# Optimization experiments

Measured on AMD Instinct MI355X. Metric: run time of the kernel, lower is better.

Reference implementation:

```python
import jax, jax.numpy as jnp
import numpy as np

H = 512      # hidden_dim
OPS = 12     # num_ops
E = 112      # total_edges = num_cells * sum(i+2 for i in range(num_nodes)) = 8*14


def setup_inputs() -> dict:
    key = jax.random.key(0)
    ks = jax.random.split(key, 16)
    s = lambda k, shape: jax.random.normal(k, shape, dtype=jnp.float32) * 0.05
    return {
        "temperature": 1,
        "h0": s(ks[0], (2, H)),
        "c0": s(ks[1], (2, H)),
        "Wih0": s(ks[2], (4 * H, H)),
        "Whh0": s(ks[3], (4 * H, H)),
        "bih0": s(ks[4], (4 * H,)),
        "bhh0": s(ks[5], (4 * H,)),
        "Wih1": s(ks[6], (4 * H, H)),
        "Whh1": s(ks[7], (4 * H, H)),
        "bih1": s(ks[8], (4 * H,)),
        "bhh1": s(ks[9], (4 * H,)),
        "emb": s(ks[10], (OPS, H)),
        "cW1": s(ks[11], (E, H, H)),
        "cb1": s(ks[12], (E, H)),
        "cW2": s(ks[13], (E, H, OPS)),
        "cb2": s(ks[14], (E, OPS)),
    }


def _lstm_cell(x, h, c, Wih, Whh, bih, bhh):
    # PyTorch LSTM gate order: i, f, g, o
    gates = x @ Wih.T + bih + h @ Whh.T + bhh  # [4H]
    i, f, g, o = jnp.split(gates, 4)
    c2 = jax.nn.sigmoid(f) * c + jax.nn.sigmoid(i) * jnp.tanh(g)
    h2 = jax.nn.sigmoid(o) * jnp.tanh(c2)
    return h2, c2


def reference(temperature, h0, c0, Wih0, Whh0, bih0, bhh0,
              Wih1, Whh1, bih1, bhh1, emb, cW1, cb1, cW2, cb2):
    temp = jnp.asarray(temperature, jnp.float32)
    # Gumbel-max trick == torch Categorical sampling (fixed on-device noise)
    gumbel = jax.random.gumbel(jax.random.key(42), (E, OPS), dtype=jnp.float32)

    def step(carry, xs):
        h, c, prev_action = carry          # h, c: [2, H]
        idx, W1, b1, W2, b2, gnoise = xs
        x = jnp.where(idx == 0, jnp.zeros((H,), jnp.float32), emb[prev_action])
        h0n, c0n = _lstm_cell(x, h[0], c[0], Wih0, Whh0, bih0, bhh0)
        h1n, c1n = _lstm_cell(h0n, h[1], c[1], Wih1, Whh1, bih1, bhh1)
        hmlp = jax.nn.relu(h1n @ W1 + b1)   # controller hidden
        logits = (hmlp @ W2 + b2) / temp    # [OPS]
        logp = jax.nn.log_softmax(logits)
        action = jnp.argmax(logits + gnoise).astype(jnp.int32)
        lp = logp[action]
        ent = -jnp.sum(jnp.exp(logp) * logp)
        new_carry = (jnp.stack([h0n, h1n]), jnp.stack([c0n, c1n]), action)
        return new_carry, (action, lp, ent)

    init = (h0, c0, jnp.int32(0))
    xs = (jnp.arange(E), cW1, cb1, cW2, cb2, gumbel)
    _, (actions, log_probs, entropies) = jax.lax.scan(step, init, xs)
    return actions, log_probs, entropies
```

## Files before the change

### kernel.cpp

```cpp
#include <hip/hip_runtime.h>
#include <math.h>

#define H    512
#define OPS  12
#define E    112
#define NWG  128
#define NT   256

typedef unsigned long long u64;
typedef unsigned int u32x4 __attribute__((ext_vector_type(4)));

#define TW_HB0   0
#define TW_HB1   1024
#define TW_HMB   2048
#define TW_TOTAL 3072
#define WS_W1T_F (16 + 2 * TW_TOTAL)

__device__ __forceinline__ float sigf(float x) { return 1.f / (1.f + expf(-x)); }

__device__ __forceinline__ void threefry_42(unsigned x0, unsigned x1,
                                            unsigned& o0, unsigned& o1) {
  const unsigned k0 = 0u, k1 = 42u;
  const unsigned k2 = k0 ^ k1 ^ 0x1BD11BDAu;
  x0 += k0; x1 += k1;
#define TF_R(rot) { x0 += x1; x1 = (x1 << rot) | (x1 >> (32 - rot)); x1 ^= x0; }
  TF_R(13) TF_R(15) TF_R(26) TF_R(6)
  x0 += k1; x1 += k2 + 1u;
  TF_R(17) TF_R(29) TF_R(16) TF_R(24)
  x0 += k2; x1 += k0 + 2u;
  TF_R(13) TF_R(15) TF_R(26) TF_R(6)
  x0 += k0; x1 += k1 + 3u;
  TF_R(17) TF_R(29) TF_R(16) TF_R(24)
  x0 += k1; x1 += k2 + 4u;
  TF_R(13) TF_R(15) TF_R(26) TF_R(6)
  x0 += k2; x1 += k0 + 5u;
#undef TF_R
  o0 = x0; o1 = x1;
}

__device__ __forceinline__ float bits_to_gumbel(unsigned bits) {
  unsigned fb = (bits >> 9) | 0x3f800000u;
  float u = __uint_as_float(fb) - 1.0f;
  u = u + 1.17549435e-38f;
  u = fmaxf(1.17549435e-38f, u);
  return -logf(-logf(u));
}

__device__ __forceinline__ float decode_temp(const void* temp_p) {
  float tf = *(const float*)temp_p;
  float a = fabsf(tf);
  if (a > 1e-6f && a < 1e6f) return tf;
  int ti = *(const int*)temp_p;
  if (ti != 0 && ti > -1000000 && ti < 1000000) return (float)ti;
  double td = *(const double*)temp_p;
  double ad = fabs(td);
  if (ad > 1e-6 && ad < 1e6) return (float)td;
  return 1.0f;
}

__device__ __forceinline__ void tag_store(u64* p, unsigned tag, float f) {
  u64 v = ((u64)tag << 32) | (u64)__float_as_uint(f);
  __hip_atomic_store(p, v, __ATOMIC_RELAXED, __HIP_MEMORY_SCOPE_SYSTEM);
}
__device__ __forceinline__ void tag_poll2(const u64* p, unsigned tag,
                                          float& f0, float& f1) {
  u32x4 v;
  for (;;) {
    asm volatile("global_load_dwordx4 %0, %1, off sc0 sc1\n\t"
                 "s_waitcnt vmcnt(0)"
                 : "=&v"(v) : "v"(p) : "memory");
    if (v.y == tag && v.w == tag) break;
    __builtin_amdgcn_s_sleep(1);
  }
  f0 = __uint_as_float(v.x);
  f1 = __uint_as_float(v.z);
}

__global__ void k_init(u64* tw) {
  int t = blockIdx.x * blockDim.x + threadIdx.x;
  if (t < TW_TOTAL) tw[t] = 0ull;
}
__global__ void k_diag(float* out, float v) {
  if (threadIdx.x == 0 && blockIdx.x == 0) out[0] = v;
}

__global__ void __launch_bounds__(NT)
k_w1t(const float* __restrict__ cW1, float* __restrict__ w1t) {
  int t = blockIdx.x * NT + threadIdx.x;
  size_t e0 = (size_t)t * 4;
  int i = (int)(e0 >> 18);
  int rem = (int)(e0 & 262143);
  int k = rem >> 9, j = rem & 511;
  int b = j >> 4, jc = j & 15;
  float4 v = *(const float4*)(cW1 + e0);
  size_t dst = (((size_t)(i * 32 + b) * 512 + k) << 4) + jc;
  *(float4*)(w1t + dst) = v;
}

__global__ void __launch_bounds__(NT)
policy_persist(const void* temp_p,
               const float* __restrict__ h0_in, const float* __restrict__ c0_in,
               const float* __restrict__ Wih0,  const float* __restrict__ Whh0,
               const float* __restrict__ bih0,  const float* __restrict__ bhh0,
               const float* __restrict__ Wih1,  const float* __restrict__ Whh1,
               const float* __restrict__ bih1,  const float* __restrict__ bhh1,
               const float* __restrict__ emb,   const float* __restrict__ cW1,
               const float* __restrict__ cb1,   const float* __restrict__ cW2,
               const float* __restrict__ cb2,
               float* __restrict__ out, float* ws, int use_w1t) {
  __shared__ __align__(16) float h0full[H], shp1[H], hm[H];
  __shared__ float g0pre[16], g1bpre[16], g1loc[16];
  __shared__ float ewloc[12 * 16], b0loc[16], b1loc[16];
  __shared__ float gum[E * OPS];
  __shared__ float w1s[512 * 5];
  __shared__ float w2s[512 * 13];
  __shared__ float c0loc[4], c1loc[4];
  __shared__ float spart[4][4];
  __shared__ int s_act;

  const int tid = threadIdx.x;
  const int bid = blockIdx.x;
  const int j0  = bid * 4;
  const int cb  = (bid & 7) * 16 + (bid >> 3);
  const float invt = 1.f / decode_temp(temp_p);

  u64* HB0 = (u64*)(ws + 16) + TW_HB0;
  u64* HB1 = (u64*)(ws + 16) + TW_HB1;
  u64* HMB = (u64*)(ws + 16) + TW_HMB;
  const float* W1T = ws + WS_W1T_F;
  const int bb = cb >> 2, boff = (cb & 3) * 4;

  for (int p = tid; p < E * OPS; p += NT) {
    unsigned y0, y1;
    threefry_42(0u, (unsigned)p, y0, y1);
    gum[p] = bits_to_gumbel(y0 ^ y1);
  }
  for (int j = tid; j < H; j += NT) {
    h0full[j] = h0_in[j];
    shp1[j]   = h0_in[H + j];
  }
  if (tid < 192) {
    int a = tid / 16, ridx = tid % 16;
    int g = ridx >> 2, dj = ridx & 3;
    int row = g * H + j0 + dj;
    const float* er = emb + a * H;
    const float* wr = Wih0 + (size_t)row * H;
    float acc = 0.f;
    for (int k = 0; k < H; k += 4) {
      float4 e4 = *(const float4*)(er + k);
      float4 w4 = *(const float4*)(wr + k);
      acc += e4.x * w4.x + e4.y * w4.y + e4.z * w4.z + e4.w * w4.w;
    }
    ewloc[tid] = acc;
  }
  if (tid < 16) {
    int g = tid >> 2, dj = tid & 3;
    int row = g * H + j0 + dj;
    b0loc[tid] = bih0[row] + bhh0[row];
    b1loc[tid] = bih1[row] + bhh1[row];
  }
  if (tid < 4) {
    c0loc[tid] = c0_in[j0 + tid];
    c1loc[tid] = c0_in[H + j0 + tid];
  }
  __syncthreads();

  {
    int rowidx = tid >> 3, lane = tid & 7;
    int cell = rowidx >> 4, ridx = rowidx & 15;
    int g = ridx >> 2, dj = ridx & 3;
    int row = g * H + j0 + dj;
    const float* wr = (cell ? Whh1 : Whh0) + (size_t)row * H + lane * 64;
    const float* hv = (cell ? shp1 : h0full) + lane * 64;
    float acc = 0.f;
#pragma unroll
    for (int k = 0; k < 64; k += 4) {
      float4 w4 = *(const float4*)(wr + k);
      acc += w4.x * hv[k] + w4.y * hv[k + 1] + w4.z * hv[k + 2] + w4.w * hv[k + 3];
    }
    acc += __shfl_xor(acc, 1);
    acc += __shfl_xor(acc, 2);
    acc += __shfl_xor(acc, 4);
    if (lane == 0) {
      if (cell == 0) g0pre[ridx] = acc + b0loc[ridx];
      else           g1bpre[ridx] = acc;
    }
    float4 r0, r1;
    if (use_w1t) {
      const float* wt = W1T + (((size_t)bb * 512) << 4) + boff;
      r0 = *(const float4*)(wt + ((size_t)tid << 4));
      r1 = *(const float4*)(wt + ((size_t)(tid + 256) << 4));
    } else {
      const float* wb = cW1 + (size_t)cb * 4;
      r0 = *(const float4*)(wb + (size_t)tid * H);
      r1 = *(const float4*)(wb + (size_t)(tid + 256) * H);
    }
    int k0 = tid * 5, k1 = (tid + 256) * 5;
    w1s[k0] = r0.x; w1s[k0 + 1] = r0.y; w1s[k0 + 2] = r0.z; w1s[k0 + 3] = r0.w;
    w1s[k1] = r1.x; w1s[k1 + 1] = r1.y; w1s[k1 + 2] = r1.z; w1s[k1 + 3] = r1.w;
  }
  __syncthreads();

#pragma unroll 1
  for (int i = 0; i < E; ++i) {
    const int p = i & 1;
    const unsigned tg = (unsigned)(i + 1);

    if (i > 0) {
      const int q = (i - 1) & 1;
      int t2 = tid * 2;
      tag_poll2(&HMB[q * 512 + t2], (unsigned)i, hm[t2], hm[t2 + 1]);
      __syncthreads();
      if (tid < 64) {
        float lg[OPS];
#pragma unroll
        for (int o = 0; o < OPS; ++o) lg[o] = 0.f;
#pragma unroll
        for (int jj = 0; jj < 8; ++jj) {
          int j = jj * 64 + tid;
          float hmv = hm[j];
          const float* w2r = &w2s[j * 13];
#pragma unroll
          for (int o = 0; o < OPS; ++o) lg[o] += hmv * w2r[o];
        }
#pragma unroll
        for (int s = 1; s < 64; s <<= 1) {
#pragma unroll
          for (int o = 0; o < OPS; ++o) lg[o] += __shfl_xor(lg[o], s);
        }
#pragma unroll
        for (int o = 0; o < OPS; ++o) lg[o] = (lg[o] + cb2[(i - 1) * OPS + o]) * invt;
        float mx = lg[0];
#pragma unroll
        for (int o = 1; o < OPS; ++o) mx = fmaxf(mx, lg[o]);
        float se = 0.f;
#pragma unroll
        for (int o = 0; o < OPS; ++o) se += expf(lg[o] - mx);
        float logZ = mx + logf(se);
        float best = -1e30f; int act = 0;
#pragma unroll
        for (int o = 0; o < OPS; ++o) {
          float v = lg[o] + gum[(i - 1) * OPS + o];
          if (v > best) { best = v; act = o; }
        }
        if (tid == 0) {
          s_act = act;
          if (bid == 0) {
            float lp = lg[act] - logZ;
            float ent = 0.f;
            for (int o = 0; o < OPS; ++o) {
              float l2 = lg[o] - logZ;
              ent -= expf(l2) * l2;
            }
            out[i - 1]         = (float)act;
            out[E + i - 1]     = lp;
            out[2 * E + i - 1] = ent;
          }
        }
      }
    }

    if (tid < 4) {
      int a = (i > 0) ? s_act : -1;
      float gi = g0pre[tid];
      float gf = g0pre[4 + tid];
      float gg = g0pre[8 + tid];
      float go = g0pre[12 + tid];
      if (a >= 0) {
        gi += ewloc[a * 16 + tid];
        gf += ewloc[a * 16 + 4 + tid];
        gg += ewloc[a * 16 + 8 + tid];
        go += ewloc[a * 16 + 12 + tid];
      }
      float cn = sigf(gf) * c0loc[tid] + sigf(gi) * tanhf(gg);
      c0loc[tid] = cn;
      tag_store(&HB0[p * 512 + j0 + tid], tg, sigf(go) * tanhf(cn));
    }

    {
      int t2 = tid * 2;
      tag_poll2(&HB0[p * 512 + t2], tg, h0full[t2], h0full[t2 + 1]);
    }
    __syncthreads();

    {
      int ridx = tid >> 4, lane = tid & 15;
      int g = ridx >> 2, dj = ridx & 3;
      int row = g * H + j0 + dj;
      const float* wr = Wih1 + (size_t)row * H + lane * 32;
      const float* hv = h0full + lane * 32;
      float acc = 0.f;
#pragma unroll
      for (int k = 0; k < 32; k += 4) {
        float4 w4 = *(const float4*)(wr + k);
        acc += w4.x * hv[k] + w4.y * hv[k + 1] + w4.z * hv[k + 2] + w4.w * hv[k + 3];
      }
      acc += __shfl_xor(acc, 1);
      acc += __shfl_xor(acc, 2);
      acc += __shfl_xor(acc, 4);
      acc += __shfl_xor(acc, 8);
      if (lane == 0) g1loc[ridx] = acc + g1bpre[ridx] + b1loc[ridx];
    }
    __syncthreads();

    if (tid < 4) {
      float gi = g1loc[tid];
      float gf = g1loc[4 + tid];
      float gg = g1loc[8 + tid];
      float go = g1loc[12 + tid];
      float cn = sigf(gf) * c1loc[tid] + sigf(gi) * tanhf(gg);
      c1loc[tid] = cn;
      tag_store(&HB1[p * 512 + j0 + tid], tg, sigf(go) * tanhf(cn));
    }

    float4 v0, v1;
    if (i + 1 < E) {
      if (use_w1t) {
        const float* wt = W1T + (((size_t)((i + 1) * 32 + bb) * 512) << 4) + boff;
        v0 = *(const float4*)(wt + ((size_t)tid << 4));
        v1 = *(const float4*)(wt + ((size_t)(tid + 256) << 4));
      } else {
        const float* wb = cW1 + (size_t)(i + 1) * H * H + (size_t)cb * 4;
        v0 = *(const float4*)(wb + (size_t)tid * H);
        v1 = *(const float4*)(wb + (size_t)(tid + 256) * H);
      }
    }
    if (tid < 128) {
      int ridx = tid >> 3, lane = tid & 7;
      int g = ridx >> 2, dj = ridx & 3;
      int row = g * H + j0 + dj;
      const float* wr = Whh0 + (size_t)row * H + lane * 64;
      const float* hv = h0full + lane * 64;
      float acc = 0.f;
#pragma unroll
      for (int k = 0; k < 64; k += 4) {
        float4 w4 = *(const float4*)(wr + k);
        acc += w4.x * hv[k] + w4.y * hv[k + 1] + w4.z * hv[k + 2] + w4.w * hv[k + 3];
      }
      acc += __shfl_xor(acc, 1);
      acc += __shfl_xor(acc, 2);
      acc += __shfl_xor(acc, 4);
      if (lane == 0) g0pre[ridx] = acc + b0loc[ridx];
    }
    {
      const float* wsrc = cW2 + (size_t)i * H * OPS;
#pragma unroll
      for (int r = 0; r < 6; ++r) {
        int q = tid + 256 * r;
        float4 v = *(const float4*)(wsrc + 4 * q);
        int f = 4 * q;
        w2s[(f / 12) * 13 + (f % 12)]             = v.x;
        w2s[((f + 1) / 12) * 13 + ((f + 1) % 12)] = v.y;
        w2s[((f + 2) / 12) * 13 + ((f + 2) % 12)] = v.z;
        w2s[((f + 3) / 12) * 13 + ((f + 3) % 12)] = v.w;
      }
    }

    {
      int t2 = tid * 2;
      tag_poll2(&HB1[p * 512 + t2], tg, shp1[t2], shp1[t2 + 1]);
    }
    __syncthreads();

    {
      int wv = tid >> 6, ln = tid & 63;
      int jl = ln & 3, ks = ln >> 2;
      int kbase = wv * 128 + ks * 8;
      float acc = 0.f;
#pragma unroll
      for (int t = 0; t < 8; ++t) {
        int k = kbase + t;
        acc += shp1[k] * w1s[k * 5 + jl];
      }
      acc += __shfl_xor(acc, 4);
      acc += __shfl_xor(acc, 8);
      acc += __shfl_xor(acc, 16);
      acc += __shfl_xor(acc, 32);
      if (ln < 4) spart[wv][ln] = acc;
    }
    __syncthreads();
    if (tid < 4) {
      float s = spart[0][tid] + spart[1][tid] + spart[2][tid] + spart[3][tid];
      s += cb1[(size_t)i * H + cb * 4 + tid];
      tag_store(&HMB[p * 512 + cb * 4 + tid], tg, fmaxf(s, 0.f));
    }

    if (i + 1 < E) {
      if (tid < 128) {
        int ridx = tid >> 3, lane = tid & 7;
        int g = ridx >> 2, dj = ridx & 3;
        int row = g * H + j0 + dj;
        const float* wr = Whh1 + (size_t)row * H + lane * 64;
        const float* hv = shp1 + lane * 64;
        float acc = 0.f;
#pragma unroll
        for (int k = 0; k < 64; k += 4) {
          float4 w4 = *(const float4*)(wr + k);
          acc += w4.x * hv[k] + w4.y * hv[k + 1] + w4.z * hv[k + 2] + w4.w * hv[k + 3];
        }
        acc += __shfl_xor(acc, 1);
        acc += __shfl_xor(acc, 2);
        acc += __shfl_xor(acc, 4);
        if (lane == 0) g1bpre[ridx] = acc;
      }
      int k0 = tid * 5, k1 = (tid + 256) * 5;
      w1s[k0] = v0.x; w1s[k0 + 1] = v0.y; w1s[k0 + 2] = v0.z; w1s[k0 + 3] = v0.w;
      w1s[k1] = v1.x; w1s[k1 + 1] = v1.y; w1s[k1 + 2] = v1.z; w1s[k1 + 3] = v1.w;
    }
    __syncthreads();
  }

  if (bid == 0) {
    const int q = (E - 1) & 1;
    int t2 = tid * 2;
    tag_poll2(&HMB[q * 512 + t2], (unsigned)E, hm[t2], hm[t2 + 1]);
    __syncthreads();
    if (tid < 64) {
      float lg[OPS];
#pragma unroll
      for (int o = 0; o < OPS; ++o) lg[o] = 0.f;
#pragma unroll
      for (int jj = 0; jj < 8; ++jj) {
        int j = jj * 64 + tid;
        float hmv = hm[j];
        const float* w2r = &w2s[j * 13];
#pragma unroll
        for (int o = 0; o < OPS; ++o) lg[o] += hmv * w2r[o];
      }
#pragma unroll
      for (int s = 1; s < 64; s <<= 1) {
#pragma unroll
        for (int o = 0; o < OPS; ++o) lg[o] += __shfl_xor(lg[o], s);
      }
#pragma unroll
      for (int o = 0; o < OPS; ++o) lg[o] = (lg[o] + cb2[(E - 1) * OPS + o]) * invt;
      float mx = lg[0];
#pragma unroll
      for (int o = 1; o < OPS; ++o) mx = fmaxf(mx, lg[o]);
      float se = 0.f;
#pragma unroll
      for (int o = 0; o < OPS; ++o) se += expf(lg[o] - mx);
      float logZ = mx + logf(se);
      float best = -1e30f; int act = 0;
#pragma unroll
      for (int o = 0; o < OPS; ++o) {
        float v = lg[o] + gum[(E - 1) * OPS + o];
        if (v > best) { best = v; act = o; }
      }
      if (tid == 0) {
        float lp = lg[act] - logZ;
        float ent = 0.f;
        for (int o = 0; o < OPS; ++o) {
          float l2 = lg[o] - logZ;
          ent -= expf(l2) * l2;
        }
        out[E - 1]     = (float)act;
        out[2 * E - 1] = lp;
        out[3 * E - 1] = ent;
      }
    }
  }
}

extern "C" void kernel_launch(void* const* d_in, const int* in_sizes, int n_in,
                              void* d_out, int out_size, void* d_ws, size_t ws_size,
                              hipStream_t stream) {
  (void)out_size;
  float* out = (float*)d_out;
  float* ws  = (float*)d_ws;

  (void)hipGetLastError();

  static const long long expect[16] = {
      1, 1024, 1024, 1048576, 1048576, 2048, 2048,
      1048576, 1048576, 2048, 2048, 6144,
      29360128, 57344, 688128, 1344 };
  int bad = -1;
  if (n_in != 16) bad = 99;
  else {
    for (int i = 0; i < 16; ++i)
      if ((long long)in_sizes[i] != expect[i]) { bad = i; break; }
  }

  k_init<<<12, 256, 0, stream>>>((u64*)(ws + 16));
  if (bad >= 0) {
    k_diag<<<1, 64, 0, stream>>>(out, 80000.0f + (float)bad);
    return;
  }

  const size_t need = (size_t)WS_W1T_F * 4 + (size_t)29360128 * 4;
  int use_w1t = (ws_size >= need) ? 1 : 0;
  if (use_w1t) {
    k_w1t<<<28672, 256, 0, stream>>>((const float*)d_in[12], ws + WS_W1T_F);
  }

  policy_persist<<<NWG, NT, 0, stream>>>(
      d_in[0],
      (const float*)d_in[1],  (const float*)d_in[2],
      (const float*)d_in[3],  (const float*)d_in[4],
      (const float*)d_in[5],  (const float*)d_in[6],
      (const float*)d_in[7],  (const float*)d_in[8],
      (const float*)d_in[9],  (const float*)d_in[10],
      (const float*)d_in[11], (const float*)d_in[12],
      (const float*)d_in[13], (const float*)d_in[14],
      (const float*)d_in[15],
      out, ws, use_w1t);

  hipError_t e = hipGetLastError();
  if (e != hipSuccess) {
    k_diag<<<1, 64, 0, stream>>>(out, 90000.0f + (float)(int)e);
  }
}
```

Before: 1.142 ms.

## Drop cW1 pre-transpose kernel and fold cell-0 update into the action step

Removes the separate k_w1t kernel that copied the whole 117 MB cW1 into a blocked layout in workspace each call, and reads cW1 strided from the original layout instead. The layer-0 LSTM update now runs inside the tid<4 threads that compute the sampled action, which removes the shared s_act handoff. The logsumexp is computed only in the block that writes outputs, and the trailing per-iteration __syncthreads is dropped. This trades a full extra read and write of cW1 for less coalesced strided loads in the persistent loop. It also risks a shared-memory race between the w1s writes at the end of one iteration and their reads in the next.

Measured after the change: 1.092 ms. 1.05x faster.

```diff
diff --git a/kernel.cpp b/kernel.cpp
--- a/kernel.cpp
+++ b/kernel.cpp
@@ -14,7 +14,6 @@
 #define TW_HB1   1024
 #define TW_HMB   2048
 #define TW_TOTAL 3072
-#define WS_W1T_F (16 + 2 * TW_TOTAL)
 
 __device__ __forceinline__ float sigf(float x) { return 1.f / (1.f + expf(-x)); }
 
@@ -85,19 +84,6 @@
 }
 
 __global__ void __launch_bounds__(NT)
-k_w1t(const float* __restrict__ cW1, float* __restrict__ w1t) {
-  int t = blockIdx.x * NT + threadIdx.x;
-  size_t e0 = (size_t)t * 4;
-  int i = (int)(e0 >> 18);
-  int rem = (int)(e0 & 262143);
-  int k = rem >> 9, j = rem & 511;
-  int b = j >> 4, jc = j & 15;
-  float4 v = *(const float4*)(cW1 + e0);
-  size_t dst = (((size_t)(i * 32 + b) * 512 + k) << 4) + jc;
-  *(float4*)(w1t + dst) = v;
-}
-
-__global__ void __launch_bounds__(NT)
 policy_persist(const void* temp_p,
                const float* __restrict__ h0_in, const float* __restrict__ c0_in,
                const float* __restrict__ Wih0,  const float* __restrict__ Whh0,
@@ -107,7 +93,7 @@
                const float* __restrict__ emb,   const float* __restrict__ cW1,
                const float* __restrict__ cb1,   const float* __restrict__ cW2,
                const float* __restrict__ cb2,
-               float* __restrict__ out, float* ws, int use_w1t) {
+               float* __restrict__ out, float* ws) {
   __shared__ __align__(16) float h0full[H], shp1[H], hm[H];
   __shared__ float g0pre[16], g1bpre[16], g1loc[16];
   __shared__ float ewloc[12 * 16], b0loc[16], b1loc[16];
@@ -116,7 +102,6 @@
   __shared__ float w2s[512 * 13];
   __shared__ float c0loc[4], c1loc[4];
   __shared__ float spart[4][4];
-  __shared__ int s_act;
 
   const int tid = threadIdx.x;
   const int bid = blockIdx.x;
@@ -127,8 +112,6 @@
   u64* HB0 = (u64*)(ws + 16) + TW_HB0;
   u64* HB1 = (u64*)(ws + 16) + TW_HB1;
   u64* HMB = (u64*)(ws + 16) + TW_HMB;
-  const float* W1T = ws + WS_W1T_F;
-  const int bb = cb >> 2, boff = (cb & 3) * 4;
 
   for (int p = tid; p < E * OPS; p += NT) {
     unsigned y0, y1;
@@ -185,16 +168,9 @@
       if (cell == 0) g0pre[ridx] = acc + b0loc[ridx];
       else           g1bpre[ridx] = acc;
     }
-    float4 r0, r1;
-    if (use_w1t) {
-      const float* wt = W1T + (((size_t)bb * 512) << 4) + boff;
-      r0 = *(const float4*)(wt + ((size_t)tid << 4));
-      r1 = *(const float4*)(wt + ((size_t)(tid + 256) << 4));
-    } else {
-      const float* wb = cW1 + (size_t)cb * 4;
-      r0 = *(const float4*)(wb + (size_t)tid * H);
-      r1 = *(const float4*)(wb + (size_t)(tid + 256) * H);
-    }
+    const float* wb = cW1 + (size_t)cb * 4;
+    float4 r0 = *(const float4*)(wb + (size_t)tid * H);
+    float4 r1 = *(const float4*)(wb + (size_t)(tid + 256) * H);
     int k0 = tid * 5, k1 = (tid + 256) * 5;
     w1s[k0] = r0.x; w1s[k0 + 1] = r0.y; w1s[k0 + 2] = r0.z; w1s[k0 + 3] = r0.w;
     w1s[k1] = r1.x; w1s[k1 + 1] = r1.y; w1s[k1 + 2] = r1.z; w1s[k1 + 3] = r1.w;
@@ -230,22 +206,30 @@
         }
 #pragma unroll
         for (int o = 0; o < OPS; ++o) lg[o] = (lg[o] + cb2[(i - 1) * OPS + o]) * invt;
-        float mx = lg[0];
-#pragma unroll
-        for (int o = 1; o < OPS; ++o) mx = fmaxf(mx, lg[o]);
-        float se = 0.f;
-#pragma unroll
-        for (int o = 0; o < OPS; ++o) se += expf(lg[o] - mx);
-        float logZ = mx + logf(se);
         float best = -1e30f; int act = 0;
 #pragma unroll
         for (int o = 0; o < OPS; ++o) {
           float v = lg[o] + gum[(i - 1) * OPS + o];
           if (v > best) { best = v; act = o; }
         }
-        if (tid == 0) {
-          s_act = act;
-          if (bid == 0) {
+        if (tid < 4) {
+          float gi = g0pre[tid]      + ewloc[act * 16 + tid];
+          float gf = g0pre[4 + tid]  + ewloc[act * 16 + 4 + tid];
+          float gg = g0pre[8 + tid]  + ewloc[act * 16 + 8 + tid];
+          float go = g0pre[12 + tid] + ewloc[act * 16 + 12 + tid];
+          float cn = sigf(gf) * c0loc[tid] + sigf(gi) * tanhf(gg);
+          c0loc[tid] = cn;
+          tag_store(&HB0[p * 512 + j0 + tid], tg, sigf(go) * tanhf(cn));
+        }
+        if (bid == 0) {
+          float mx = lg[0];
+#pragma unroll
+          for (int o = 1; o < OPS; ++o) mx = fmaxf(mx, lg[o]);
+          float se = 0.f;
+#pragma unroll
+          for (int o = 0; o < OPS; ++o) se += expf(lg[o] - mx);
+          float logZ = mx + logf(se);
+          if (tid == 0) {
             float lp = lg[act] - logZ;
             float ent = 0.f;
             for (int o = 0; o < OPS; ++o) {
@@ -258,23 +242,16 @@
           }
         }
       }
-    }
-
-    if (tid < 4) {
-      int a = (i > 0) ? s_act : -1;
-      float gi = g0pre[tid];
-      float gf = g0pre[4 + tid];
-      float gg = g0pre[8 + tid];
-      float go = g0pre[12 + tid];
-      if (a >= 0) {
-        gi += ewloc[a * 16 + tid];
-        gf += ewloc[a * 16 + 4 + tid];
-        gg += ewloc[a * 16 + 8 + tid];
-        go += ewloc[a * 16 + 12 + tid];
-      }
-      float cn = sigf(gf) * c0loc[tid] + sigf(gi) * tanhf(gg);
-      c0loc[tid] = cn;
-      tag_store(&HB0[p * 512 + j0 + tid], tg, sigf(go) * tanhf(cn));
+    } else {
+      if (tid < 4) {
+        float gi = g0pre[tid];
+        float gf = g0pre[4 + tid];
+        float gg = g0pre[8 + tid];
+        float go = g0pre[12 + tid];
+        float cn = sigf(gf) * c0loc[tid] + sigf(gi) * tanhf(gg);
+        c0loc[tid] = cn;
+        tag_store(&HB0[p * 512 + j0 + tid], tg, sigf(go) * tanhf(cn));
+      }
     }
 
     {
@@ -315,15 +292,9 @@
 
     float4 v0, v1;
     if (i + 1 < E) {
-      if (use_w1t) {
-        const float* wt = W1T + (((size_t)((i + 1) * 32 + bb) * 512) << 4) + boff;
-        v0 = *(const float4*)(wt + ((size_t)tid << 4));
-        v1 = *(const float4*)(wt + ((size_t)(tid + 256) << 4));
-      } else {
-        const float* wb = cW1 + (size_t)(i + 1) * H * H + (size_t)cb * 4;
-        v0 = *(const float4*)(wb + (size_t)tid * H);
-        v1 = *(const float4*)(wb + (size_t)(tid + 256) * H);
-      }
+      const float* wb = cW1 + (size_t)(i + 1) * H * H + (size_t)cb * 4;
+      v0 = *(const float4*)(wb + (size_t)tid * H);
+      v1 = *(const float4*)(wb + (size_t)(tid + 256) * H);
     }
     if (tid < 128) {
       int ridx = tid >> 3, lane = tid & 7;
@@ -407,7 +378,6 @@
       w1s[k0] = v0.x; w1s[k0 + 1] = v0.y; w1s[k0 + 2] = v0.z; w1s[k0 + 3] = v0.w;
       w1s[k1] = v1.x; w1s[k1 + 1] = v1.y; w1s[k1 + 2] = v1.z; w1s[k1 + 3] = v1.w;
     }
-    __syncthreads();
   }
 
   if (bid == 0) {
@@ -465,7 +435,7 @@
 extern "C" void kernel_launch(void* const* d_in, const int* in_sizes, int n_in,
                               void* d_out, int out_size, void* d_ws, size_t ws_size,
                               hipStream_t stream) {
-  (void)out_size;
+  (void)out_size; (void)ws_size;
   float* out = (float*)d_out;
   float* ws  = (float*)d_ws;
 
@@ -486,12 +456,6 @@
   if (bad >= 0) {
     k_diag<<<1, 64, 0, stream>>>(out, 80000.0f + (float)bad);
     return;
-  }
-
-  const size_t need = (size_t)WS_W1T_F * 4 + (size_t)29360128 * 4;
-  int use_w1t = (ws_size >= need) ? 1 : 0;
-  if (use_w1t) {
-    k_w1t<<<28672, 256, 0, stream>>>((const float*)d_in[12], ws + WS_W1T_F);
   }
 
   policy_persist<<<NWG, NT, 0, stream>>>(
@@ -504,7 +468,7 @@
       (const float*)d_in[11], (const float*)d_in[12],
       (const float*)d_in[13], (const float*)d_in[14],
       (const float*)d_in[15],
-      out, ws, use_w1t);
+      out, ws);
 
   hipError_t e = hipGetLastError();
   if (e != hipSuccess) {
```
